# Kernel tuning notes

Hardware: AMD Instinct MI355X
Metric: run time of the kernel (lower is better)

## Reference

```python
import jax, jax.numpy as jnp
import numpy as np

# Complete binary tree: node 0 is the root, node i's parent is (i-1)//2.
# adjacency[i, j] = 1 iff j is the parent of i (matches _parent_indices/_child_indices).
N_LEVELS = 11
N_LABELS = 2 ** N_LEVELS - 1  # 2047
N_CLASSES = 2
BATCH = 2048


def _tree_structure():
    # levels[t]: node ids at tree level t (root level 0)
    levels = [np.arange(2 ** t - 1, 2 ** (t + 1) - 1) for t in range(N_LEVELS)]
    parent = np.zeros(N_LABELS, dtype=np.int64)
    parent[1:] = (np.arange(1, N_LABELS) - 1) // 2
    return levels, parent


def _propagate(emissions, transitions, edge_layers):
    """Belief-propagation sweep. edge_layers is a list (per depth, in order)
    of (src, dst) numpy index arrays: each src node sends a message to dst.
    Message: m[b, c_dst, dst] += logsumexp_{c_src}(emissions[b,c_src,src]
              + messages[b,c_src,src] + transitions[dst, src, c_dst, c_src]).
    Identical math to (Batched)MessagePassing.forward, expressed per edge.
    """
    messages = jnp.zeros_like(emissions)
    for src, dst in edge_layers:
        e = emissions[:, :, src] + messages[:, :, src]           # [B, Cs, E]
        t = transitions[dst, src]                                 # [E, Cd, Cs]
        # elem[b, cd, e, cs] = e[b, cs, e] + t[e, cd, cs]
        elem = e.transpose(0, 2, 1)[:, None, :, :] + t.transpose(1, 0, 2)[None]
        contrib = jax.nn.logsumexp(elem, axis=-1)                 # [B, Cd, E]
        messages = messages.at[:, :, dst].add(contrib)
    return messages


def setup_inputs() -> dict:
    key = jax.random.key(0)
    k1, k2 = jax.random.split(key)
    emissions = jax.random.normal(k1, (BATCH, N_CLASSES, N_LABELS), dtype=jnp.float32)
    transitions = jax.random.normal(k2, (N_LABELS, N_LABELS, N_CLASSES, N_CLASSES), dtype=jnp.float32)
    return {"emissions": emissions, "transitions": transitions}


def reference(emissions, transitions):
    levels, parent = _tree_structure()
    # upward (alphas): leaves -> root, successor = parent
    up_edges = [(levels[t], parent[levels[t]]) for t in range(N_LEVELS - 1, 0, -1)]
    # downward (betas): root -> leaves, successor = child
    down_edges = [(parent[levels[t]], levels[t]) for t in range(1, N_LEVELS)]
    alphas = _propagate(emissions, transitions, up_edges)
    betas = _propagate(emissions, transitions, down_edges)
    scores = emissions + alphas + betas                           # [B, C, L]
    # normalize over classes per label -> marginal log-probabilities
    return scores - jax.nn.logsumexp(scores, axis=1, keepdims=True)
```

## Files before the change

### kernel.cpp

```cpp
#include <hip/hip_runtime.h>


#define L 2047
#define NSLOTS 78

typedef float __attribute__((ext_vector_type(4), aligned(4))) uf4;
typedef float __attribute__((ext_vector_type(2), aligned(4))) uf2;

__device__ __forceinline__ float lse2(float x, float y) {
    float m = fmaxf(x, y);
    return m + __logf(1.0f + __expf(fminf(x, y) - m));
}

__device__ __forceinline__ void up_pair(float c00, float c01, float c10, float c11,
                                        float4 tA, float4 tB, float em0, float em1,
                                        float& o0, float& o1) {
    o0 = em0 + lse2(c00 + tA.x, c01 + tA.y) + lse2(c10 + tB.x, c11 + tB.y);
    o1 = em1 + lse2(c00 + tA.z, c01 + tA.w) + lse2(c10 + tB.z, c11 + tB.w);
}

__device__ __forceinline__ void slot_decode(int s, int l, int& node, int& src) {
    if (s < 16)      { int p = 511 + 8*l + (s >> 1); node = p; src = 2*p + 1 + (s & 1); }
    else if (s < 24) { int j = s - 16; int p = 255 + 4*l + (j >> 1); node = p; src = 2*p + 1 + (j & 1); }
    else if (s < 28) { int j = s - 24; int p = 127 + 2*l + (j >> 1); node = p; src = 2*p + 1 + (j & 1); }
    else if (s < 30) { int j = s - 28; int p = 63 + l; node = p; src = 2*p + 1 + j; }
    else if (s < 42) { int d = (s - 30) >> 1; int r = (s - 30) & 1;
                       int P = (1 << (5 - d)) - 1 + (l >> (d + 1)); node = P; src = 2*P + 1 + r; }
    else if (s < 47) { int t = s - 41; int n = (1 << t) - 1 + (l >> (6 - t)); node = n; src = (n - 1) >> 1; }
    else if (s < 48) { int n = 63 + l; node = n; src = (n - 1) >> 1; }
    else if (s < 50) { int j = s - 48; int n = 127 + 2*l + j; node = n; src = (n - 1) >> 1; }
    else if (s < 54) { int j = s - 50; int n = 255 + 4*l + j; node = n; src = (n - 1) >> 1; }
    else if (s < 62) { int j = s - 54; int n = 511 + 8*l + j; node = n; src = (n - 1) >> 1; }
    else             { int j = s - 62; int n = 1023 + 16*l + j; node = n; src = (n - 1) >> 1; }
}

__device__ __forceinline__ float4 ldT(const float4* __restrict__ pk,
                                      const float4* __restrict__ tr4, int s, int l) {
    if (pk) return pk[(s << 6) + l];
    int n, c; slot_decode(s, l, n, c);
    return tr4[n * L + c];
}

__global__ void pack_kernel(const float4* __restrict__ tr4, float4* __restrict__ packed) {
    int idx = blockIdx.x * 256 + threadIdx.x;
    if (idx >= NSLOTS * 64) return;
    int s = idx >> 6, l = idx & 63;
    int n, c; slot_decode(s, l, n, c);
    packed[idx] = tr4[n * L + c];
}

__global__ __launch_bounds__(64) void treecrf_main(
    const float* __restrict__ emissions,
    const float4* __restrict__ pk,
    const float4* __restrict__ tr4,
    float* __restrict__ out)
{
    const int l = threadIdx.x;
    const int b = blockIdx.x;
    const float* __restrict__ e0 = emissions + (size_t)b * (2 * L);
    const float* __restrict__ e1 = e0 + L;
    float* __restrict__ o0 = out + (size_t)b * (2 * L);
    float* __restrict__ o1 = o0 + L;

    float el0[16], el1[16];
    {
        const uf4* p0 = (const uf4*)(e0 + 1023 + 16 * l);
        const uf4* p1 = (const uf4*)(e1 + 1023 + 16 * l);
        #pragma unroll
        for (int k = 0; k < 4; ++k) {
            uf4 a = p0[k], c = p1[k];
            el0[4*k] = a.x; el0[4*k+1] = a.y; el0[4*k+2] = a.z; el0[4*k+3] = a.w;
            el1[4*k] = c.x; el1[4*k+1] = c.y; el1[4*k+2] = c.z; el1[4*k+3] = c.w;
        }
    }
    float em9_0[8], em9_1[8], em8_0[4], em8_1[4], em7_0[2], em7_1[2], em6_0, em6_1;
    {
        const uf4* p0 = (const uf4*)(e0 + 511 + 8 * l);
        const uf4* p1 = (const uf4*)(e1 + 511 + 8 * l);
        uf4 a = p0[0], bq = p0[1], c = p1[0], d = p1[1];
        em9_0[0]=a.x; em9_0[1]=a.y; em9_0[2]=a.z; em9_0[3]=a.w;
        em9_0[4]=bq.x; em9_0[5]=bq.y; em9_0[6]=bq.z; em9_0[7]=bq.w;
        em9_1[0]=c.x; em9_1[1]=c.y; em9_1[2]=c.z; em9_1[3]=c.w;
        em9_1[4]=d.x; em9_1[5]=d.y; em9_1[6]=d.z; em9_1[7]=d.w;
        uf4 e = *(const uf4*)(e0 + 255 + 4 * l);
        uf4 f = *(const uf4*)(e1 + 255 + 4 * l);
        em8_0[0]=e.x; em8_0[1]=e.y; em8_0[2]=e.z; em8_0[3]=e.w;
        em8_1[0]=f.x; em8_1[1]=f.y; em8_1[2]=f.z; em8_1[3]=f.w;
        uf2 g = *(const uf2*)(e0 + 127 + 2 * l);
        uf2 h = *(const uf2*)(e1 + 127 + 2 * l);
        em7_0[0]=g.x; em7_0[1]=g.y; em7_1[0]=h.x; em7_1[1]=h.y;
        em6_0 = e0[63 + l]; em6_1 = e1[63 + l];
    }

    float A9_0[8], A9_1[8];
    #pragma unroll
    for (int j = 0; j < 8; ++j) {
        float4 tA = ldT(pk, tr4, 2*j, l), tB = ldT(pk, tr4, 2*j + 1, l);
        up_pair(el0[2*j], el1[2*j], el0[2*j+1], el1[2*j+1], tA, tB,
                em9_0[j], em9_1[j], A9_0[j], A9_1[j]);
    }
    float A8_0[4], A8_1[4];
    #pragma unroll
    for (int j = 0; j < 4; ++j) {
        float4 tA = ldT(pk, tr4, 16 + 2*j, l), tB = ldT(pk, tr4, 17 + 2*j, l);
        up_pair(A9_0[2*j], A9_1[2*j], A9_0[2*j+1], A9_1[2*j+1], tA, tB,
                em8_0[j], em8_1[j], A8_0[j], A8_1[j]);
    }
    float A7_0[2], A7_1[2];
    #pragma unroll
    for (int j = 0; j < 2; ++j) {
        float4 tA = ldT(pk, tr4, 24 + 2*j, l), tB = ldT(pk, tr4, 25 + 2*j, l);
        up_pair(A8_0[2*j], A8_1[2*j], A8_0[2*j+1], A8_1[2*j+1], tA, tB,
                em7_0[j], em7_1[j], A7_0[j], A7_1[j]);
    }
    float A6_0, A6_1;
    {
        float4 tA = ldT(pk, tr4, 28, l), tB = ldT(pk, tr4, 29, l);
        up_pair(A7_0[0], A7_1[0], A7_0[1], A7_1[1], tA, tB, em6_0, em6_1, A6_0, A6_1);
    }

    float cur0 = A6_0, cur1 = A6_1;
    float Aa0[6], Aa1[6], Ea0[6], Ea1[6];
    #pragma unroll
    for (int d = 0; d < 6; ++d) {
        const int t = 5 - d;
        const int P = (1 << t) - 1 + (l >> (d + 1));
        float p0v = __shfl_xor(cur0, 1 << d);
        float p1v = __shfl_xor(cur1, 1 << d);
        bool isL = ((l >> d) & 1) == 0;
        float L0 = isL ? cur0 : p0v, L1 = isL ? cur1 : p1v;
        float R0 = isL ? p0v : cur0, R1 = isL ? p1v : cur1;
        float4 tL = ldT(pk, tr4, 30 + 2*d, l), tR = ldT(pk, tr4, 31 + 2*d, l);
        float eP0 = e0[P], eP1 = e1[P];
        up_pair(L0, L1, R0, R1, tL, tR, eP0, eP1, cur0, cur1);
        Aa0[t] = cur0; Aa1[t] = cur1; Ea0[t] = eP0; Ea1[t] = eP1;
    }

    if (l == 0) {
        float m = lse2(cur0, cur1);
        o0[0] = cur0 - m; o1[0] = cur1 - m;
    }
    float D0 = Ea0[0], D1 = Ea1[0];

    #pragma unroll
    for (int t = 1; t <= 5; ++t) {
        const int n = (1 << t) - 1 + (l >> (6 - t));
        float4 td = ldT(pk, tr4, 41 + t, l);
        float b0 = lse2(D0 + td.x, D1 + td.y);
        float b1 = lse2(D0 + td.z, D1 + td.w);
        float s0 = Aa0[t] + b0, s1 = Aa1[t] + b1;
        float m = lse2(s0, s1);
        if ((l & ((1 << (6 - t)) - 1)) == 0) { o0[n] = s0 - m; o1[n] = s1 - m; }
        D0 = Ea0[t] + b0; D1 = Ea1[t] + b1;
    }

    {
        float4 td = ldT(pk, tr4, 47, l);
        float b0 = lse2(D0 + td.x, D1 + td.y);
        float b1 = lse2(D0 + td.z, D1 + td.w);
        float s0 = A6_0 + b0, s1 = A6_1 + b1, m = lse2(s0, s1);
        o0[63 + l] = s0 - m; o1[63 + l] = s1 - m;
        D0 = em6_0 + b0; D1 = em6_1 + b1;
    }

    float D7_0[2], D7_1[2];
    {
        float w0[2], w1[2];
        #pragma unroll
        for (int j = 0; j < 2; ++j) {
            float4 td = ldT(pk, tr4, 48 + j, l);
            float b0 = lse2(D0 + td.x, D1 + td.y);
            float b1 = lse2(D0 + td.z, D1 + td.w);
            float s0 = A7_0[j] + b0, s1 = A7_1[j] + b1, m = lse2(s0, s1);
            w0[j] = s0 - m; w1[j] = s1 - m;
            D7_0[j] = em7_0[j] + b0; D7_1[j] = em7_1[j] + b1;
        }
        *(uf2*)(o0 + 127 + 2*l) = uf2{w0[0], w0[1]};
        *(uf2*)(o1 + 127 + 2*l) = uf2{w1[0], w1[1]};
    }

    float D8_0[4], D8_1[4];
    {
        float w0[4], w1[4];
        #pragma unroll
        for (int j = 0; j < 4; ++j) {
            float4 td = ldT(pk, tr4, 50 + j, l);
            float b0 = lse2(D7_0[j>>1] + td.x, D7_1[j>>1] + td.y);
            float b1 = lse2(D7_0[j>>1] + td.z, D7_1[j>>1] + td.w);
            float s0 = A8_0[j] + b0, s1 = A8_1[j] + b1, m = lse2(s0, s1);
            w0[j] = s0 - m; w1[j] = s1 - m;
            D8_0[j] = em8_0[j] + b0; D8_1[j] = em8_1[j] + b1;
        }
        *(uf4*)(o0 + 255 + 4*l) = uf4{w0[0], w0[1], w0[2], w0[3]};
        *(uf4*)(o1 + 255 + 4*l) = uf4{w1[0], w1[1], w1[2], w1[3]};
    }

    float D9_0[8], D9_1[8];
    {
        float w0[8], w1[8];
        #pragma unroll
        for (int j = 0; j < 8; ++j) {
            float4 td = ldT(pk, tr4, 54 + j, l);
            float b0 = lse2(D8_0[j>>1] + td.x, D8_1[j>>1] + td.y);
            float b1 = lse2(D8_0[j>>1] + td.z, D8_1[j>>1] + td.w);
            float s0 = A9_0[j] + b0, s1 = A9_1[j] + b1, m = lse2(s0, s1);
            w0[j] = s0 - m; w1[j] = s1 - m;
            D9_0[j] = em9_0[j] + b0; D9_1[j] = em9_1[j] + b1;
        }
        uf4* q0 = (uf4*)(o0 + 511 + 8*l);
        uf4* q1 = (uf4*)(o1 + 511 + 8*l);
        q0[0] = uf4{w0[0], w0[1], w0[2], w0[3]}; q0[1] = uf4{w0[4], w0[5], w0[6], w0[7]};
        q1[0] = uf4{w1[0], w1[1], w1[2], w1[3]}; q1[1] = uf4{w1[4], w1[5], w1[6], w1[7]};
    }

    {
        float w0[16], w1[16];
        #pragma unroll
        for (int k = 0; k < 16; ++k) {
            float4 td = ldT(pk, tr4, 62 + k, l);
            float b0 = lse2(D9_0[k>>1] + td.x, D9_1[k>>1] + td.y);
            float b1 = lse2(D9_0[k>>1] + td.z, D9_1[k>>1] + td.w);
            float s0 = el0[k] + (A9_0[k>>1] - em9_0[k>>1], 0.f), s1;
            s0 = el0[k] + b0; s1 = el1[k] + b1;
            float m = lse2(s0, s1);
            w0[k] = s0 - m; w1[k] = s1 - m;
        }
        uf4* q0 = (uf4*)(o0 + 1023 + 16*l);
        uf4* q1 = (uf4*)(o1 + 1023 + 16*l);
        #pragma unroll
        for (int k = 0; k < 4; ++k) {
            q0[k] = uf4{w0[4*k], w0[4*k+1], w0[4*k+2], w0[4*k+3]};
            q1[k] = uf4{w1[4*k], w1[4*k+1], w1[4*k+2], w1[4*k+3]};
        }
    }
}

extern "C" void kernel_launch(void* const* d_in, const int* in_sizes, int n_in,
                              void* d_out, int out_size, void* d_ws, size_t ws_size,
                              hipStream_t stream) {
    const float* emissions = (const float*)d_in[0];
    const float4* tr4 = (const float4*)d_in[1];
    float* out = (float*)d_out;

    const size_t packed_bytes = (size_t)NSLOTS * 64 * sizeof(float4);
    const bool use_ws = (ws_size >= packed_bytes) && (d_ws != nullptr);
    float4* pk = use_ws ? (float4*)d_ws : nullptr;
    if (use_ws) {
        pack_kernel<<<(NSLOTS * 64 + 255) / 256, 256, 0, stream>>>(tr4, pk);
    }
    treecrf_main<<<2048, 64, 0, stream>>>(emissions, pk, tr4, out);
}
```

Baseline: 138.5 us.

## Stage packed transitions in LDS shared by four batch rows per block

Each block now serves four batch elements (256 threads) and cooperatively loads 62 of the 78 packed transition slots into shared memory, so four wavefronts share one copy instead of each reading it from global/L2. The first 16 slots go into registers per thread, and the emission loads for the ancestor nodes are moved earlier so their latency overlaps the leaf stage. The cost is about 62KB of LDS per block, which limits how many blocks fit per CU, plus a block-wide barrier and more register pressure from holding 16 float4s.

```diff
diff --git a/kernel.cpp b/kernel.cpp
--- a/kernel.cpp
+++ b/kernel.cpp
@@ -3,6 +3,8 @@
 
 #define L 2047
 #define NSLOTS 78
+#define S0 16
+#define NLDS (NSLOTS - S0)
 
 typedef float __attribute__((ext_vector_type(4), aligned(4))) uf4;
 typedef float __attribute__((ext_vector_type(2), aligned(4))) uf2;
@@ -34,13 +36,6 @@
     else             { int j = s - 62; int n = 1023 + 16*l + j; node = n; src = (n - 1) >> 1; }
 }
 
-__device__ __forceinline__ float4 ldT(const float4* __restrict__ pk,
-                                      const float4* __restrict__ tr4, int s, int l) {
-    if (pk) return pk[(s << 6) + l];
-    int n, c; slot_decode(s, l, n, c);
-    return tr4[n * L + c];
-}
-
 __global__ void pack_kernel(const float4* __restrict__ tr4, float4* __restrict__ packed) {
     int idx = blockIdx.x * 256 + threadIdx.x;
     if (idx >= NSLOTS * 64) return;
@@ -49,18 +44,47 @@
     packed[idx] = tr4[n * L + c];
 }
 
-__global__ __launch_bounds__(64) void treecrf_main(
+__global__ __launch_bounds__(256) void treecrf_main(
     const float* __restrict__ emissions,
     const float4* __restrict__ pk,
     const float4* __restrict__ tr4,
     float* __restrict__ out)
 {
-    const int l = threadIdx.x;
-    const int b = blockIdx.x;
+    __shared__ float4 lt[NLDS * 64];
+
+    const int tid = threadIdx.x;
+    const int l = tid & 63;
+    const int b = blockIdx.x * 4 + (tid >> 6);
     const float* __restrict__ e0 = emissions + (size_t)b * (2 * L);
     const float* __restrict__ e1 = e0 + L;
     float* __restrict__ o0 = out + (size_t)b * (2 * L);
     float* __restrict__ o1 = o0 + L;
+
+    if (pk) {
+        #pragma unroll
+        for (int k = 0; k < 16; ++k) {
+            int i = tid + k * 256;
+            if (i < NLDS * 64) lt[i] = pk[S0 * 64 + i];
+        }
+    } else {
+        for (int i = tid; i < NLDS * 64; i += 256) {
+            int n, c; slot_decode(S0 + (i >> 6), i & 63, n, c);
+            lt[i] = tr4[n * L + c];
+        }
+    }
+    #define LT(s) lt[(((s) - S0) << 6) + l]
+
+    float4 t9[16];
+    if (pk) {
+        #pragma unroll
+        for (int k = 0; k < 16; ++k) t9[k] = pk[(k << 6) + l];
+    } else {
+        #pragma unroll
+        for (int k = 0; k < 16; ++k) {
+            int n, c; slot_decode(k, l, n, c);
+            t9[k] = tr4[n * L + c];
+        }
+    }
 
     float el0[16], el1[16];
     {
@@ -91,49 +115,47 @@
         em7_0[0]=g.x; em7_0[1]=g.y; em7_1[0]=h.x; em7_1[1]=h.y;
         em6_0 = e0[63 + l]; em6_1 = e1[63 + l];
     }
+    float Ea0[6], Ea1[6];
+    #pragma unroll
+    for (int t = 0; t <= 5; ++t) {
+        const int P = (1 << t) - 1 + (l >> (6 - t));
+        Ea0[t] = e0[P]; Ea1[t] = e1[P];
+    }
 
     float A9_0[8], A9_1[8];
     #pragma unroll
-    for (int j = 0; j < 8; ++j) {
-        float4 tA = ldT(pk, tr4, 2*j, l), tB = ldT(pk, tr4, 2*j + 1, l);
-        up_pair(el0[2*j], el1[2*j], el0[2*j+1], el1[2*j+1], tA, tB,
+    for (int j = 0; j < 8; ++j)
+        up_pair(el0[2*j], el1[2*j], el0[2*j+1], el1[2*j+1], t9[2*j], t9[2*j+1],
                 em9_0[j], em9_1[j], A9_0[j], A9_1[j]);
-    }
+
+    __syncthreads();
+
     float A8_0[4], A8_1[4];
     #pragma unroll
-    for (int j = 0; j < 4; ++j) {
-        float4 tA = ldT(pk, tr4, 16 + 2*j, l), tB = ldT(pk, tr4, 17 + 2*j, l);
-        up_pair(A9_0[2*j], A9_1[2*j], A9_0[2*j+1], A9_1[2*j+1], tA, tB,
-                em8_0[j], em8_1[j], A8_0[j], A8_1[j]);
-    }
+    for (int j = 0; j < 4; ++j)
+        up_pair(A9_0[2*j], A9_1[2*j], A9_0[2*j+1], A9_1[2*j+1],
+                LT(16 + 2*j), LT(17 + 2*j), em8_0[j], em8_1[j], A8_0[j], A8_1[j]);
     float A7_0[2], A7_1[2];
     #pragma unroll
-    for (int j = 0; j < 2; ++j) {
-        float4 tA = ldT(pk, tr4, 24 + 2*j, l), tB = ldT(pk, tr4, 25 + 2*j, l);
-        up_pair(A8_0[2*j], A8_1[2*j], A8_0[2*j+1], A8_1[2*j+1], tA, tB,
-                em7_0[j], em7_1[j], A7_0[j], A7_1[j]);
-    }
+    for (int j = 0; j < 2; ++j)
+        up_pair(A8_0[2*j], A8_1[2*j], A8_0[2*j+1], A8_1[2*j+1],
+                LT(24 + 2*j), LT(25 + 2*j), em7_0[j], em7_1[j], A7_0[j], A7_1[j]);
     float A6_0, A6_1;
-    {
-        float4 tA = ldT(pk, tr4, 28, l), tB = ldT(pk, tr4, 29, l);
-        up_pair(A7_0[0], A7_1[0], A7_0[1], A7_1[1], tA, tB, em6_0, em6_1, A6_0, A6_1);
-    }
+    up_pair(A7_0[0], A7_1[0], A7_0[1], A7_1[1], LT(28), LT(29), em6_0, em6_1, A6_0, A6_1);
 
     float cur0 = A6_0, cur1 = A6_1;
-    float Aa0[6], Aa1[6], Ea0[6], Ea1[6];
+    float Aa0[6], Aa1[6];
     #pragma unroll
     for (int d = 0; d < 6; ++d) {
         const int t = 5 - d;
-        const int P = (1 << t) - 1 + (l >> (d + 1));
         float p0v = __shfl_xor(cur0, 1 << d);
         float p1v = __shfl_xor(cur1, 1 << d);
         bool isL = ((l >> d) & 1) == 0;
-        float L0 = isL ? cur0 : p0v, L1 = isL ? cur1 : p1v;
-        float R0 = isL ? p0v : cur0, R1 = isL ? p1v : cur1;
-        float4 tL = ldT(pk, tr4, 30 + 2*d, l), tR = ldT(pk, tr4, 31 + 2*d, l);
-        float eP0 = e0[P], eP1 = e1[P];
-        up_pair(L0, L1, R0, R1, tL, tR, eP0, eP1, cur0, cur1);
-        Aa0[t] = cur0; Aa1[t] = cur1; Ea0[t] = eP0; Ea1[t] = eP1;
+        float Lc0 = isL ? cur0 : p0v, Lc1 = isL ? cur1 : p1v;
+        float Rc0 = isL ? p0v : cur0, Rc1 = isL ? p1v : cur1;
+        float4 tL = LT(30 + 2*d), tR = LT(31 + 2*d);
+        up_pair(Lc0, Lc1, Rc0, Rc1, tL, tR, Ea0[t], Ea1[t], cur0, cur1);
+        Aa0[t] = cur0; Aa1[t] = cur1;
     }
 
     if (l == 0) {
@@ -145,17 +167,16 @@
     #pragma unroll
     for (int t = 1; t <= 5; ++t) {
         const int n = (1 << t) - 1 + (l >> (6 - t));
-        float4 td = ldT(pk, tr4, 41 + t, l);
+        float4 td = LT(41 + t);
         float b0 = lse2(D0 + td.x, D1 + td.y);
         float b1 = lse2(D0 + td.z, D1 + td.w);
-        float s0 = Aa0[t] + b0, s1 = Aa1[t] + b1;
-        float m = lse2(s0, s1);
+        float s0 = Aa0[t] + b0, s1 = Aa1[t] + b1, m = lse2(s0, s1);
         if ((l & ((1 << (6 - t)) - 1)) == 0) { o0[n] = s0 - m; o1[n] = s1 - m; }
         D0 = Ea0[t] + b0; D1 = Ea1[t] + b1;
     }
 
     {
-        float4 td = ldT(pk, tr4, 47, l);
+        float4 td = LT(47);
         float b0 = lse2(D0 + td.x, D1 + td.y);
         float b1 = lse2(D0 + td.z, D1 + td.w);
         float s0 = A6_0 + b0, s1 = A6_1 + b1, m = lse2(s0, s1);
@@ -168,7 +189,7 @@
         float w0[2], w1[2];
         #pragma unroll
         for (int j = 0; j < 2; ++j) {
-            float4 td = ldT(pk, tr4, 48 + j, l);
+            float4 td = LT(48 + j);
             float b0 = lse2(D0 + td.x, D1 + td.y);
             float b1 = lse2(D0 + td.z, D1 + td.w);
             float s0 = A7_0[j] + b0, s1 = A7_1[j] + b1, m = lse2(s0, s1);
@@ -184,7 +205,7 @@
         float w0[4], w1[4];
         #pragma unroll
         for (int j = 0; j < 4; ++j) {
-            float4 td = ldT(pk, tr4, 50 + j, l);
+            float4 td = LT(50 + j);
             float b0 = lse2(D7_0[j>>1] + td.x, D7_1[j>>1] + td.y);
             float b1 = lse2(D7_0[j>>1] + td.z, D7_1[j>>1] + td.w);
             float s0 = A8_0[j] + b0, s1 = A8_1[j] + b1, m = lse2(s0, s1);
@@ -200,7 +221,7 @@
         float w0[8], w1[8];
         #pragma unroll
         for (int j = 0; j < 8; ++j) {
-            float4 td = ldT(pk, tr4, 54 + j, l);
+            float4 td = LT(54 + j);
             float b0 = lse2(D8_0[j>>1] + td.x, D8_1[j>>1] + td.y);
             float b1 = lse2(D8_0[j>>1] + td.z, D8_1[j>>1] + td.w);
             float s0 = A9_0[j] + b0, s1 = A9_1[j] + b1, m = lse2(s0, s1);
@@ -217,12 +238,10 @@
         float w0[16], w1[16];
         #pragma unroll
         for (int k = 0; k < 16; ++k) {
-            float4 td = ldT(pk, tr4, 62 + k, l);
+            float4 td = LT(62 + k);
             float b0 = lse2(D9_0[k>>1] + td.x, D9_1[k>>1] + td.y);
             float b1 = lse2(D9_0[k>>1] + td.z, D9_1[k>>1] + td.w);
-            float s0 = el0[k] + (A9_0[k>>1] - em9_0[k>>1], 0.f), s1;
-            s0 = el0[k] + b0; s1 = el1[k] + b1;
-            float m = lse2(s0, s1);
+            float s0 = el0[k] + b0, s1 = el1[k] + b1, m = lse2(s0, s1);
             w0[k] = s0 - m; w1[k] = s1 - m;
         }
         uf4* q0 = (uf4*)(o0 + 1023 + 16*l);
@@ -233,6 +252,7 @@
             q1[k] = uf4{w1[4*k], w1[4*k+1], w1[4*k+2], w1[4*k+3]};
         }
     }
+    #undef LT
 }
 
 extern "C" void kernel_launch(void* const* d_in, const int* in_sizes, int n_in,
@@ -245,8 +265,7 @@
     const size_t packed_bytes = (size_t)NSLOTS * 64 * sizeof(float4);
     const bool use_ws = (ws_size >= packed_bytes) && (d_ws != nullptr);
     float4* pk = use_ws ? (float4*)d_ws : nullptr;
-    if (use_ws) {
+    if (use_ws)
         pack_kernel<<<(NSLOTS * 64 + 255) / 256, 256, 0, stream>>>(tr4, pk);
-    }
-    treecrf_main<<<2048, 64, 0, stream>>>(emissions, pk, tr4, out);
-}
+    treecrf_main<<<512, 256, 0, stream>>>(emissions, pk, tr4, out);
+}
```

Measured after the change: 135.8 us. 2.0% less time.

## Split each batch row across two wavefronts, one per root subtree

Applied to the files above, without the earlier changes.

Each block now runs 128 threads, and each 64-lane wavefront handles one of the root's two subtrees, so every thread owns half as many leaves. The two subtree root alphas are exchanged through shared memory with a barrier to compute the root. Per-thread register arrays and serial work shrink, which should help latency and occupancy. The cost is a block-level sync, a duplicated downward pass near the root, and a larger packed transition table. The kernel is also templated on whether packed transitions are used, removing a runtime branch.

```diff
diff --git a/kernel.cpp b/kernel.cpp
--- a/kernel.cpp
+++ b/kernel.cpp
@@ -2,7 +2,8 @@
 
 
 #define L 2047
-#define NSLOTS 78
+#define NSLOT 49
+#define PK_ELEMS (2 * NSLOT * 64)
 
 typedef float __attribute__((ext_vector_type(4), aligned(4))) uf4;
 typedef float __attribute__((ext_vector_type(2), aligned(4))) uf2;
@@ -19,219 +20,194 @@
     o1 = em1 + lse2(c00 + tA.z, c01 + tA.w) + lse2(c10 + tB.z, c11 + tB.w);
 }
 
-__device__ __forceinline__ void slot_decode(int s, int l, int& node, int& src) {
-    if (s < 16)      { int p = 511 + 8*l + (s >> 1); node = p; src = 2*p + 1 + (s & 1); }
-    else if (s < 24) { int j = s - 16; int p = 255 + 4*l + (j >> 1); node = p; src = 2*p + 1 + (j & 1); }
-    else if (s < 28) { int j = s - 24; int p = 127 + 2*l + (j >> 1); node = p; src = 2*p + 1 + (j & 1); }
-    else if (s < 30) { int j = s - 28; int p = 63 + l; node = p; src = 2*p + 1 + j; }
-    else if (s < 42) { int d = (s - 30) >> 1; int r = (s - 30) & 1;
-                       int P = (1 << (5 - d)) - 1 + (l >> (d + 1)); node = P; src = 2*P + 1 + r; }
-    else if (s < 47) { int t = s - 41; int n = (1 << t) - 1 + (l >> (6 - t)); node = n; src = (n - 1) >> 1; }
-    else if (s < 48) { int n = 63 + l; node = n; src = (n - 1) >> 1; }
-    else if (s < 50) { int j = s - 48; int n = 127 + 2*l + j; node = n; src = (n - 1) >> 1; }
-    else if (s < 54) { int j = s - 50; int n = 255 + 4*l + j; node = n; src = (n - 1) >> 1; }
-    else if (s < 62) { int j = s - 54; int n = 511 + 8*l + j; node = n; src = (n - 1) >> 1; }
-    else             { int j = s - 62; int n = 1023 + 16*l + j; node = n; src = (n - 1) >> 1; }
-}
-
-__device__ __forceinline__ float4 ldT(const float4* __restrict__ pk,
-                                      const float4* __restrict__ tr4, int s, int l) {
-    if (pk) return pk[(s << 6) + l];
-    int n, c; slot_decode(s, l, n, c);
-    return tr4[n * L + c];
-}
-
-__global__ void pack_kernel(const float4* __restrict__ tr4, float4* __restrict__ packed) {
+__device__ __forceinline__ void slot_decode(int r, int s, int l, int& dst, int& src) {
+    const int n7 = 127 + 64 * r + l;
+    if (s < 8)       { int k = s >> 1;      dst = 4*n7 + 3 + k;         src = 2*dst + 1 + (s & 1); }
+    else if (s < 12) { int j = (s - 8) >> 1;dst = 2*n7 + 1 + j;         src = 2*dst + 1 + (s & 1); }
+    else if (s < 14) {                      dst = n7;                   src = 2*n7 + 1 + (s - 12); }
+    else if (s < 26) { int d = (s - 14) >> 1; dst = ((n7+1) >> (d+1)) - 1; src = 2*dst + 1 + (s & 1); }
+    else if (s < 28) {                      dst = 0;                    src = 1 + (s - 26); }
+    else if (s < 34) { int t = s - 27;      dst = ((n7+1) >> (7-t)) - 1; src = (dst - 1) >> 1; }
+    else if (s < 35) {                      dst = n7;                   src = (n7 - 1) >> 1; }
+    else if (s < 37) {                      dst = 2*n7 + 1 + (s - 35);  src = n7; }
+    else if (s < 41) {                      dst = 4*n7 + 3 + (s - 37);  src = (dst - 1) >> 1; }
+    else             {                      dst = 8*n7 + 7 + (s - 41);  src = (dst - 1) >> 1; }
+}
+
+__global__ void pack_kernel(const float4* __restrict__ tr4, float4* __restrict__ pk) {
     int idx = blockIdx.x * 256 + threadIdx.x;
-    if (idx >= NSLOTS * 64) return;
-    int s = idx >> 6, l = idx & 63;
-    int n, c; slot_decode(s, l, n, c);
-    packed[idx] = tr4[n * L + c];
-}
-
-__global__ __launch_bounds__(64) void treecrf_main(
+    if (idx >= PK_ELEMS) return;
+    int r = idx / (NSLOT * 64);
+    int rem = idx - r * (NSLOT * 64);
+    int s = rem >> 6, l = rem & 63;
+    int d_, c_; slot_decode(r, s, l, d_, c_);
+    pk[idx] = tr4[d_ * L + c_];
+}
+
+template <bool UPK>
+__global__ __launch_bounds__(128, 4) void treecrf_main(
     const float* __restrict__ emissions,
     const float4* __restrict__ pk,
     const float4* __restrict__ tr4,
     float* __restrict__ out)
 {
-    const int l = threadIdx.x;
+    __shared__ float sh[4];
+    const int tid = threadIdx.x;
+    const int l = tid & 63;
+    const int r = tid >> 6;
     const int b = blockIdx.x;
     const float* __restrict__ e0 = emissions + (size_t)b * (2 * L);
     const float* __restrict__ e1 = e0 + L;
     float* __restrict__ o0 = out + (size_t)b * (2 * L);
     float* __restrict__ o1 = o0 + L;
 
-    float el0[16], el1[16];
-    {
-        const uf4* p0 = (const uf4*)(e0 + 1023 + 16 * l);
-        const uf4* p1 = (const uf4*)(e1 + 1023 + 16 * l);
-        #pragma unroll
-        for (int k = 0; k < 4; ++k) {
-            uf4 a = p0[k], c = p1[k];
-            el0[4*k] = a.x; el0[4*k+1] = a.y; el0[4*k+2] = a.z; el0[4*k+3] = a.w;
-            el1[4*k] = c.x; el1[4*k+1] = c.y; el1[4*k+2] = c.z; el1[4*k+3] = c.w;
-        }
-    }
-    float em9_0[8], em9_1[8], em8_0[4], em8_1[4], em7_0[2], em7_1[2], em6_0, em6_1;
-    {
-        const uf4* p0 = (const uf4*)(e0 + 511 + 8 * l);
-        const uf4* p1 = (const uf4*)(e1 + 511 + 8 * l);
-        uf4 a = p0[0], bq = p0[1], c = p1[0], d = p1[1];
+    auto FL = [&](int s) -> float4 {
+        if (UPK) return pk[((r * NSLOT + s) << 6) + l];
+        int d_, c_; slot_decode(r, s, l, d_, c_);
+        return tr4[d_ * L + c_];
+    };
+
+    float el0[8], el1[8];
+    {
+        const uf4* p0 = (const uf4*)(e0 + 1023 + 512*r + 8*l);
+        const uf4* p1 = (const uf4*)(e1 + 1023 + 512*r + 8*l);
+        uf4 a = p0[0], c = p0[1], d = p1[0], e = p1[1];
+        el0[0]=a.x; el0[1]=a.y; el0[2]=a.z; el0[3]=a.w;
+        el0[4]=c.x; el0[5]=c.y; el0[6]=c.z; el0[7]=c.w;
+        el1[0]=d.x; el1[1]=d.y; el1[2]=d.z; el1[3]=d.w;
+        el1[4]=e.x; el1[5]=e.y; el1[6]=e.z; el1[7]=e.w;
+    }
+    float em9_0[4], em9_1[4], em8_0[2], em8_1[2], em7_0, em7_1;
+    {
+        uf4 a = *(const uf4*)(e0 + 511 + 256*r + 4*l);
+        uf4 c = *(const uf4*)(e1 + 511 + 256*r + 4*l);
         em9_0[0]=a.x; em9_0[1]=a.y; em9_0[2]=a.z; em9_0[3]=a.w;
-        em9_0[4]=bq.x; em9_0[5]=bq.y; em9_0[6]=bq.z; em9_0[7]=bq.w;
         em9_1[0]=c.x; em9_1[1]=c.y; em9_1[2]=c.z; em9_1[3]=c.w;
-        em9_1[4]=d.x; em9_1[5]=d.y; em9_1[6]=d.z; em9_1[7]=d.w;
-        uf4 e = *(const uf4*)(e0 + 255 + 4 * l);
-        uf4 f = *(const uf4*)(e1 + 255 + 4 * l);
-        em8_0[0]=e.x; em8_0[1]=e.y; em8_0[2]=e.z; em8_0[3]=e.w;
-        em8_1[0]=f.x; em8_1[1]=f.y; em8_1[2]=f.z; em8_1[3]=f.w;
-        uf2 g = *(const uf2*)(e0 + 127 + 2 * l);
-        uf2 h = *(const uf2*)(e1 + 127 + 2 * l);
-        em7_0[0]=g.x; em7_0[1]=g.y; em7_1[0]=h.x; em7_1[1]=h.y;
-        em6_0 = e0[63 + l]; em6_1 = e1[63 + l];
-    }
-
-    float A9_0[8], A9_1[8];
-    #pragma unroll
-    for (int j = 0; j < 8; ++j) {
-        float4 tA = ldT(pk, tr4, 2*j, l), tB = ldT(pk, tr4, 2*j + 1, l);
-        up_pair(el0[2*j], el1[2*j], el0[2*j+1], el1[2*j+1], tA, tB,
-                em9_0[j], em9_1[j], A9_0[j], A9_1[j]);
-    }
-    float A8_0[4], A8_1[4];
-    #pragma unroll
-    for (int j = 0; j < 4; ++j) {
-        float4 tA = ldT(pk, tr4, 16 + 2*j, l), tB = ldT(pk, tr4, 17 + 2*j, l);
-        up_pair(A9_0[2*j], A9_1[2*j], A9_0[2*j+1], A9_1[2*j+1], tA, tB,
+        uf2 g = *(const uf2*)(e0 + 255 + 128*r + 2*l);
+        uf2 h = *(const uf2*)(e1 + 255 + 128*r + 2*l);
+        em8_0[0]=g.x; em8_0[1]=g.y; em8_1[0]=h.x; em8_1[1]=h.y;
+        em7_0 = e0[127 + 64*r + l]; em7_1 = e1[127 + 64*r + l];
+    }
+    float Ea0[7], Ea1[7];
+    Ea0[0] = e0[0]; Ea1[0] = e1[0];
+    #pragma unroll
+    for (int t = 1; t <= 6; ++t) {
+        const int n = ((128 + 64*r + l) >> (7 - t)) - 1;
+        Ea0[t] = e0[n]; Ea1[t] = e1[n];
+    }
+
+    float A9_0[4], A9_1[4];
+    #pragma unroll
+    for (int k = 0; k < 4; ++k)
+        up_pair(el0[2*k], el1[2*k], el0[2*k+1], el1[2*k+1], FL(2*k), FL(2*k+1),
+                em9_0[k], em9_1[k], A9_0[k], A9_1[k]);
+    float A8_0[2], A8_1[2];
+    #pragma unroll
+    for (int j = 0; j < 2; ++j)
+        up_pair(A9_0[2*j], A9_1[2*j], A9_0[2*j+1], A9_1[2*j+1], FL(8+2*j), FL(9+2*j),
                 em8_0[j], em8_1[j], A8_0[j], A8_1[j]);
-    }
-    float A7_0[2], A7_1[2];
-    #pragma unroll
-    for (int j = 0; j < 2; ++j) {
-        float4 tA = ldT(pk, tr4, 24 + 2*j, l), tB = ldT(pk, tr4, 25 + 2*j, l);
-        up_pair(A8_0[2*j], A8_1[2*j], A8_0[2*j+1], A8_1[2*j+1], tA, tB,
-                em7_0[j], em7_1[j], A7_0[j], A7_1[j]);
-    }
-    float A6_0, A6_1;
-    {
-        float4 tA = ldT(pk, tr4, 28, l), tB = ldT(pk, tr4, 29, l);
-        up_pair(A7_0[0], A7_1[0], A7_0[1], A7_1[1], tA, tB, em6_0, em6_1, A6_0, A6_1);
-    }
-
-    float cur0 = A6_0, cur1 = A6_1;
-    float Aa0[6], Aa1[6], Ea0[6], Ea1[6];
+    float A7_0, A7_1;
+    up_pair(A8_0[0], A8_1[0], A8_0[1], A8_1[1], FL(12), FL(13), em7_0, em7_1, A7_0, A7_1);
+
+    float cur0 = A7_0, cur1 = A7_1;
+    float Aa0[7], Aa1[7];
     #pragma unroll
     for (int d = 0; d < 6; ++d) {
-        const int t = 5 - d;
-        const int P = (1 << t) - 1 + (l >> (d + 1));
+        const int t = 6 - d;
         float p0v = __shfl_xor(cur0, 1 << d);
         float p1v = __shfl_xor(cur1, 1 << d);
         bool isL = ((l >> d) & 1) == 0;
-        float L0 = isL ? cur0 : p0v, L1 = isL ? cur1 : p1v;
-        float R0 = isL ? p0v : cur0, R1 = isL ? p1v : cur1;
-        float4 tL = ldT(pk, tr4, 30 + 2*d, l), tR = ldT(pk, tr4, 31 + 2*d, l);
-        float eP0 = e0[P], eP1 = e1[P];
-        up_pair(L0, L1, R0, R1, tL, tR, eP0, eP1, cur0, cur1);
-        Aa0[t] = cur0; Aa1[t] = cur1; Ea0[t] = eP0; Ea1[t] = eP1;
-    }
-
-    if (l == 0) {
-        float m = lse2(cur0, cur1);
-        o0[0] = cur0 - m; o1[0] = cur1 - m;
-    }
+        float Lc0 = isL ? cur0 : p0v, Lc1 = isL ? cur1 : p1v;
+        float Rc0 = isL ? p0v : cur0, Rc1 = isL ? p1v : cur1;
+        up_pair(Lc0, Lc1, Rc0, Rc1, FL(14 + 2*d), FL(15 + 2*d),
+                Ea0[t], Ea1[t], cur0, cur1);
+        Aa0[t] = cur0; Aa1[t] = cur1;
+    }
+
+    if (l == 0) { sh[2*r] = cur0; sh[2*r + 1] = cur1; }
+    __syncthreads();
+    {
+        float a1_0 = sh[0], a1_1 = sh[1], a2_0 = sh[2], a2_1 = sh[3];
+        float4 t1 = FL(26), t2 = FL(27);
+        float AR0 = Ea0[0] + lse2(a1_0 + t1.x, a1_1 + t1.y)
+                           + lse2(a2_0 + t2.x, a2_1 + t2.y);
+        float AR1 = Ea1[0] + lse2(a1_0 + t1.z, a1_1 + t1.w)
+                           + lse2(a2_0 + t2.z, a2_1 + t2.w);
+        if (r == 0 && l == 0) {
+            float m = lse2(AR0, AR1);
+            o0[0] = AR0 - m; o1[0] = AR1 - m;
+        }
+    }
+
     float D0 = Ea0[0], D1 = Ea1[0];
-
-    #pragma unroll
-    for (int t = 1; t <= 5; ++t) {
-        const int n = (1 << t) - 1 + (l >> (6 - t));
-        float4 td = ldT(pk, tr4, 41 + t, l);
+    #pragma unroll
+    for (int t = 1; t <= 6; ++t) {
+        float4 td = FL(27 + t);
         float b0 = lse2(D0 + td.x, D1 + td.y);
         float b1 = lse2(D0 + td.z, D1 + td.w);
-        float s0 = Aa0[t] + b0, s1 = Aa1[t] + b1;
-        float m = lse2(s0, s1);
-        if ((l & ((1 << (6 - t)) - 1)) == 0) { o0[n] = s0 - m; o1[n] = s1 - m; }
+        float s0 = Aa0[t] + b0, s1 = Aa1[t] + b1, m = lse2(s0, s1);
+        if ((l & ((1 << (7 - t)) - 1)) == 0) {
+            const int n = ((128 + 64*r + l) >> (7 - t)) - 1;
+            o0[n] = s0 - m; o1[n] = s1 - m;
+        }
         D0 = Ea0[t] + b0; D1 = Ea1[t] + b1;
     }
 
     {
-        float4 td = ldT(pk, tr4, 47, l);
+        float4 td = FL(34);
         float b0 = lse2(D0 + td.x, D1 + td.y);
         float b1 = lse2(D0 + td.z, D1 + td.w);
-        float s0 = A6_0 + b0, s1 = A6_1 + b1, m = lse2(s0, s1);
-        o0[63 + l] = s0 - m; o1[63 + l] = s1 - m;
-        D0 = em6_0 + b0; D1 = em6_1 + b1;
-    }
-
-    float D7_0[2], D7_1[2];
+        float s0 = A7_0 + b0, s1 = A7_1 + b1, m = lse2(s0, s1);
+        o0[127 + 64*r + l] = s0 - m; o1[127 + 64*r + l] = s1 - m;
+        D0 = em7_0 + b0; D1 = em7_1 + b1;
+    }
+
+    float D8_0[2], D8_1[2];
     {
         float w0[2], w1[2];
         #pragma unroll
         for (int j = 0; j < 2; ++j) {
-            float4 td = ldT(pk, tr4, 48 + j, l);
+            float4 td = FL(35 + j);
             float b0 = lse2(D0 + td.x, D1 + td.y);
             float b1 = lse2(D0 + td.z, D1 + td.w);
-            float s0 = A7_0[j] + b0, s1 = A7_1[j] + b1, m = lse2(s0, s1);
-            w0[j] = s0 - m; w1[j] = s1 - m;
-            D7_0[j] = em7_0[j] + b0; D7_1[j] = em7_1[j] + b1;
-        }
-        *(uf2*)(o0 + 127 + 2*l) = uf2{w0[0], w0[1]};
-        *(uf2*)(o1 + 127 + 2*l) = uf2{w1[0], w1[1]};
-    }
-
-    float D8_0[4], D8_1[4];
-    {
-        float w0[4], w1[4];
-        #pragma unroll
-        for (int j = 0; j < 4; ++j) {
-            float4 td = ldT(pk, tr4, 50 + j, l);
-            float b0 = lse2(D7_0[j>>1] + td.x, D7_1[j>>1] + td.y);
-            float b1 = lse2(D7_0[j>>1] + td.z, D7_1[j>>1] + td.w);
             float s0 = A8_0[j] + b0, s1 = A8_1[j] + b1, m = lse2(s0, s1);
             w0[j] = s0 - m; w1[j] = s1 - m;
             D8_0[j] = em8_0[j] + b0; D8_1[j] = em8_1[j] + b1;
         }
-        *(uf4*)(o0 + 255 + 4*l) = uf4{w0[0], w0[1], w0[2], w0[3]};
-        *(uf4*)(o1 + 255 + 4*l) = uf4{w1[0], w1[1], w1[2], w1[3]};
-    }
-
-    float D9_0[8], D9_1[8];
+        *(uf2*)(o0 + 255 + 128*r + 2*l) = uf2{w0[0], w0[1]};
+        *(uf2*)(o1 + 255 + 128*r + 2*l) = uf2{w1[0], w1[1]};
+    }
+
+    float D9_0[4], D9_1[4];
+    {
+        float w0[4], w1[4];
+        #pragma unroll
+        for (int k = 0; k < 4; ++k) {
+            float4 td = FL(37 + k);
+            float b0 = lse2(D8_0[k>>1] + td.x, D8_1[k>>1] + td.y);
+            float b1 = lse2(D8_0[k>>1] + td.z, D8_1[k>>1] + td.w);
+            float s0 = A9_0[k] + b0, s1 = A9_1[k] + b1, m = lse2(s0, s1);
+            w0[k] = s0 - m; w1[k] = s1 - m;
+            D9_0[k] = em9_0[k] + b0; D9_1[k] = em9_1[k] + b1;
+        }
+        *(uf4*)(o0 + 511 + 256*r + 4*l) = uf4{w0[0], w0[1], w0[2], w0[3]};
+        *(uf4*)(o1 + 511 + 256*r + 4*l) = uf4{w1[0], w1[1], w1[2], w1[3]};
+    }
+
     {
         float w0[8], w1[8];
         #pragma unroll
-        for (int j = 0; j < 8; ++j) {
-            float4 td = ldT(pk, tr4, 54 + j, l);
-            float b0 = lse2(D8_0[j>>1] + td.x, D8_1[j>>1] + td.y);
-            float b1 = lse2(D8_0[j>>1] + td.z, D8_1[j>>1] + td.w);
-            float s0 = A9_0[j] + b0, s1 = A9_1[j] + b1, m = lse2(s0, s1);
-            w0[j] = s0 - m; w1[j] = s1 - m;
-            D9_0[j] = em9_0[j] + b0; D9_1[j] = em9_1[j] + b1;
-        }
-        uf4* q0 = (uf4*)(o0 + 511 + 8*l);
-        uf4* q1 = (uf4*)(o1 + 511 + 8*l);
+        for (int m2 = 0; m2 < 8; ++m2) {
+            float4 td = FL(41 + m2);
+            float b0 = lse2(D9_0[m2>>1] + td.x, D9_1[m2>>1] + td.y);
+            float b1 = lse2(D9_0[m2>>1] + td.z, D9_1[m2>>1] + td.w);
+            float s0 = el0[m2] + b0, s1 = el1[m2] + b1, m = lse2(s0, s1);
+            w0[m2] = s0 - m; w1[m2] = s1 - m;
+        }
+        uf4* q0 = (uf4*)(o0 + 1023 + 512*r + 8*l);
+        uf4* q1 = (uf4*)(o1 + 1023 + 512*r + 8*l);
         q0[0] = uf4{w0[0], w0[1], w0[2], w0[3]}; q0[1] = uf4{w0[4], w0[5], w0[6], w0[7]};
         q1[0] = uf4{w1[0], w1[1], w1[2], w1[3]}; q1[1] = uf4{w1[4], w1[5], w1[6], w1[7]};
-    }
-
-    {
-        float w0[16], w1[16];
-        #pragma unroll
-        for (int k = 0; k < 16; ++k) {
-            float4 td = ldT(pk, tr4, 62 + k, l);
-            float b0 = lse2(D9_0[k>>1] + td.x, D9_1[k>>1] + td.y);
-            float b1 = lse2(D9_0[k>>1] + td.z, D9_1[k>>1] + td.w);
-            float s0 = el0[k] + (A9_0[k>>1] - em9_0[k>>1], 0.f), s1;
-            s0 = el0[k] + b0; s1 = el1[k] + b1;
-            float m = lse2(s0, s1);
-            w0[k] = s0 - m; w1[k] = s1 - m;
-        }
-        uf4* q0 = (uf4*)(o0 + 1023 + 16*l);
-        uf4* q1 = (uf4*)(o1 + 1023 + 16*l);
-        #pragma unroll
-        for (int k = 0; k < 4; ++k) {
-            q0[k] = uf4{w0[4*k], w0[4*k+1], w0[4*k+2], w0[4*k+3]};
-            q1[k] = uf4{w1[4*k], w1[4*k+1], w1[4*k+2], w1[4*k+3]};
-        }
     }
 }
 
@@ -242,11 +218,13 @@
     const float4* tr4 = (const float4*)d_in[1];
     float* out = (float*)d_out;
 
-    const size_t packed_bytes = (size_t)NSLOTS * 64 * sizeof(float4);
+    const size_t packed_bytes = (size_t)PK_ELEMS * sizeof(float4);
     const bool use_ws = (ws_size >= packed_bytes) && (d_ws != nullptr);
-    float4* pk = use_ws ? (float4*)d_ws : nullptr;
     if (use_ws) {
-        pack_kernel<<<(NSLOTS * 64 + 255) / 256, 256, 0, stream>>>(tr4, pk);
-    }
-    treecrf_main<<<2048, 64, 0, stream>>>(emissions, pk, tr4, out);
-}
+        float4* pk = (float4*)d_ws;
+        pack_kernel<<<(PK_ELEMS + 255) / 256, 256, 0, stream>>>(tr4, pk);
+        treecrf_main<true><<<2048, 128, 0, stream>>>(emissions, pk, tr4, out);
+    } else {
+        treecrf_main<false><<<2048, 128, 0, stream>>>(emissions, nullptr, tr4, out);
+    }
+}
```

After: 133.5 us. -3.6%, faster.
